# Kernel tuning notes

Hardware: AMD Instinct MI355X
Metric: run time of the kernel (lower is better)

Reference implementation:

```python
import jax, jax.numpy as jnp
import numpy as np

B, N, NB, E, H, A, K, D = 32, 512, 10, 1024, 256, 82, 4, 3


def setup_inputs() -> dict:
    key = jax.random.key(0)
    ks = iter(jax.random.split(key, 64))
    f = lambda shape: jax.random.normal(next(ks), shape, jnp.float32) * 0.05
    inp = {
        "atom_fea": jax.random.normal(next(ks), (B, N, A), jnp.float32),
        "bond_fea": jax.random.normal(next(ks), (B, E, 6), jnp.float32),
        "d_anb": jax.random.randint(next(ks), (B, N, NB), 0, N),
        "d_bnb": jax.random.randint(next(ks), (B, N, NB), 0, E),
        "d_nbs_mask": (jax.random.uniform(next(ks), (B, N, NB)) < 0.8).astype(jnp.float32),
        "d_mask": (jax.random.uniform(next(ks), (B, N)) < 0.9).astype(jnp.float32),
        "Wv": f((A, H)), "bv": f((H,)),
        "Wa_main": f((D, K, H, H)), "ba_main": f((D, K, H)),
        "Wa_super": f((D, K, H, H)), "ba_super": f((D, K, H)),
        "Wm": f((D, K, H, H)), "bm": f((D, K, H)),
        "Wbmm": f((D, K, H)), "bbmm": f((D, K)),
        "Wm2s": f((D, K * H, H)), "bm2s": f((D, H)),
        "Ws2m": f((D, H, H)), "bs2m": f((D, H)),
        "Wsup": f((D, H, H)), "bsup": f((D, H)),
        "Wzm1": f((D, H, H)), "bzm1": f((D, H)),
        "Wzm2": f((D, H, H)), "bzm2": f((D, H)),
        "Wzs1": f((D, H, H)), "bzs1": f((D, H)),
        "Wzs2": f((D, H, H)), "bzs2": f((D, H)),
        "Wu2": f((D, H + 6, H)), "bu2": f((D, H)),
        "Wu1": f((D, 2 * H, H)), "bu1": f((D, H)),
    }
    return inp


def mask_softmax(a, mask):
    a_max = jnp.max(a, -1, keepdims=True)
    e = jnp.exp(a - a_max) * mask
    return e / (jnp.sum(e, -1, keepdims=True) + 1e-6)


def _forward(atom_fea, bond_fea, d_nbs_mask, d_mask,
             Wv, bv, Wa_main, ba_main, Wa_super, ba_super, Wm, bm, Wbmm, bbmm,
             Wm2s, bm2s, Ws2m, bs2m, Wsup, bsup,
             Wzm1, bzm1, Wzm2, bzm2, Wzs1, bzs1, Wzs2, bzs2,
             Wu2, bu2, Wu1, bu1, d_anb, d_bnb):
    Bn = atom_fea.shape[0]
    bidx = jnp.arange(Bn)[:, None, None]
    # vertex embedding (default leaky_relu slope 0.01)
    vf = jax.nn.leaky_relu(atom_fea @ Wv + bv, 0.01)            # [B,N,H]
    sf = jnp.sum(vf * d_mask[:, :, None], axis=1, keepdims=True)  # [B,1,H]
    mask3 = d_nbs_mask[..., None]                               # [B,N,NB,1]
    for d in range(D):
        # --- multi-head main->super attention (vectorized over heads k) ---
        a_main = jnp.tanh(jnp.einsum('bnh,khj->bknj', vf, Wa_main[d]) + ba_main[d][None, :, None, :])
        a_super = jnp.tanh(jnp.einsum('boh,khj->bkoj', sf, Wa_super[d]) + ba_super[d][None, :, None, :])
        a = jnp.einsum('bknh,kh->bkn', a_main * a_super, Wbmm[d]) + bbmm[d][None, :, None]
        attn = mask_softmax(a, d_mask[:, None, :])               # [B,K,N]
        mvf = jnp.einsum('bnh,khj->bknj', vf, Wm[d]) + bm[d][None, :, None, :]
        m2s = jnp.einsum('bkn,bknh->bkh', attn, mvf).reshape(Bn, 1, K * H)
        main_to_super = jnp.tanh(m2s @ Wm2s[d] + bm2s[d])        # [B,1,H]
        # --- wln unit: gather neighbors, MLP, masked sum (slope 0.1) ---
        vnei = vf[bidx, d_anb]                                   # [B,N,NB,H]
        enei = bond_fea[bidx, d_bnb]                             # [B,N,NB,6]
        lnei = jnp.concatenate([vnei, enei], -1)                 # [B,N,NB,H+6]
        nei = jax.nn.leaky_relu(lnei @ Wu2[d] + bu2[d], 0.1)
        nei = jnp.sum(nei * mask3, axis=2)                       # [B,N,H]
        main_self = jax.nn.leaky_relu(jnp.concatenate([vf, nei], -1) @ Wu1[d] + bu1[d], 0.1)
        # --- GRU-style gated updates ---
        super_to_main = jnp.tanh(sf @ Ws2m[d] + bs2m[d])         # [B,1,H]
        super_self = jnp.tanh(sf @ Wsup[d] + bsup[d])            # [B,1,H]
        z_main = jax.nn.sigmoid(main_self @ Wzm1[d] + bzm1[d] + super_to_main @ Wzm2[d] + bzm2[d])
        vf = (1 - z_main) * main_self + z_main * super_to_main
        z_sup = jax.nn.sigmoid(super_self @ Wzs1[d] + bzs1[d] + main_to_super @ Wzs2[d] + bzs2[d])
        sf = (1 - z_sup) * super_self + z_sup * main_to_super    # [B,1,H]; sum over dim 1 is a no-op
    return vf, sf


def reference(atom_fea, bond_fea, d_anb, d_bnb, d_nbs_mask, d_mask,
              Wv, bv, Wa_main, ba_main, Wa_super, ba_super, Wm, bm, Wbmm, bbmm,
              Wm2s, bm2s, Ws2m, bs2m, Wsup, bsup,
              Wzm1, bzm1, Wzm2, bzm2, Wzs1, bzs1, Wzs2, bzs2,
              Wu2, bu2, Wu1, bu1):
    return _forward(atom_fea, bond_fea, d_nbs_mask, d_mask,
                    Wv, bv, Wa_main, ba_main, Wa_super, ba_super, Wm, bm, Wbmm, bbmm,
                    Wm2s, bm2s, Ws2m, bs2m, Wsup, bsup,
                    Wzm1, bzm1, Wzm2, bzm2, Wzs1, bzs1, Wzs2, bzs2,
                    Wu2, bu2, Wu1, bu1, d_anb, d_bnb)
```

## Files before the change

kernel.cpp:

```cpp
#include <hip/hip_runtime.h>
#include <hip/hip_bf16.h>

#define B_ 32
#define N_ 512
#define NB_ 10
#define E_ 1024
#define H_ 256
#define A_ 82
#define K_ 4
#define D_ 3
#define M_ (B_*N_)

typedef unsigned short u16;
typedef __attribute__((ext_vector_type(8))) short bf16x8;
typedef __attribute__((ext_vector_type(4))) float f32x4;

__device__ __forceinline__ float b2f(u16 u){
    unsigned int x = ((unsigned int)u) << 16;
    return __builtin_bit_cast(float, x);
}
__device__ __forceinline__ u16 f2b(float f){
    unsigned int x = __builtin_bit_cast(unsigned int, f);
    unsigned int lsb = (x >> 16) & 1u;
    x += 0x7fffu + lsb;
    return (u16)(x >> 16);
}
__device__ __forceinline__ float sigmoidf_(float x){ return 1.f/(1.f+expf(-x)); }

static constexpr int CVT_N[31] = {
    B_*E_*6, B_*N_*NB_, B_*N_,
    A_*H_, H_,
    D_*K_*H_*H_, D_*K_*H_, D_*K_*H_*H_, D_*K_*H_,
    D_*K_*H_*H_, D_*K_*H_, D_*K_*H_, D_*K_,
    D_*K_*H_*H_, D_*H_, D_*H_*H_, D_*H_,
    D_*H_*H_, D_*H_, D_*H_*H_, D_*H_,
    D_*H_*H_, D_*H_, D_*H_*H_, D_*H_,
    D_*H_*H_, D_*H_, D_*(H_+6)*H_, D_*H_,
    D_*2*H_*H_, D_*H_
};
struct Offs { long v[32]; };
static constexpr Offs mk_offs(){
    Offs o{}; o.v[0]=0;
    for(int i=0;i<31;i++) o.v[i+1]=o.v[i]+CVT_N[i];
    return o;
}
static constexpr Offs CVT_OFF = mk_offs();

struct Ptrs { const void* p[31]; };

__global__ void k_detect(const unsigned short* __restrict__ wv_raw, int* __restrict__ flag){
    float v = b2f(wv_raw[threadIdx.x]);
    bool plaus = (v==v) && (fabsf(v) < 100.0f);
    unsigned long long m = __ballot(plaus);
    if (threadIdx.x==0) *flag = (m == ~0ULL) ? 1 : 0;
}

__global__ void k_cvt(Ptrs ptrs, float* __restrict__ dst, const int* __restrict__ flag){
    int t = blockIdx.y;
    int n = CVT_N[t];
    int i4 = blockIdx.x*256 + threadIdx.x;
    if (i4*4 >= n) return;
    const void* src = ptrs.p[t];
    float4 o;
    if (*flag){
        ushort4 u = ((const ushort4*)src)[i4];
        o.x=b2f(u.x); o.y=b2f(u.y); o.z=b2f(u.z); o.w=b2f(u.w);
    } else {
        o = ((const float4*)src)[i4];
    }
    *(float4*)(dst + CVT_OFF.v[t] + (size_t)i4*4) = o;
}

__global__ void k_wt(const float* __restrict__ Wam, const float* __restrict__ Wu2,
                     const float* __restrict__ Wu1, const float* __restrict__ Wzm1,
                     u16* __restrict__ WT){
    int mi = blockIdx.z;
    const float* src;
    if (mi<12)      src = Wam  + (size_t)mi*H_*H_;
    else if (mi<15) src = Wu2  + (size_t)(mi-12)*(H_+6)*H_;
    else if (mi<18) src = Wu1  + (size_t)(mi-15)*2*H_*H_;
    else if (mi<21) src = Wu1  + (size_t)(mi-18)*2*H_*H_ + (size_t)H_*H_;
    else            src = Wzm1 + (size_t)(mi-21)*H_*H_;
    __shared__ float t[32][33];
    int x = threadIdx.x, y = threadIdx.y;
    int k0 = blockIdx.y*32, n0 = blockIdx.x*32;
    for(int yy=y; yy<32; yy+=8) t[yy][x] = src[(size_t)(k0+yy)*H_ + n0+x];
    __syncthreads();
    u16* dst = WT + ((size_t)mi*8 + (k0>>5))*(256*32);
    for(int yy=y; yy<32; yy+=8) dst[(size_t)(n0+yy)*32 + x] = f2b(t[x][yy]);
}

__global__ void k_embed(const u16* __restrict__ atom, const float* __restrict__ Wv,
                        const float* __restrict__ bv, u16* __restrict__ vfb,
                        const int* __restrict__ flag){
    __shared__ float arow[8][A_];
    int r0 = blockIdx.x*8; int j = threadIdx.x;
    int fl = *flag;
    for(int i=j;i<8*A_;i+=256){
        int r=i/A_, a=i-r*A_;
        arow[r][a] = fl ? b2f(atom[(size_t)(r0+r)*A_+a])
                        : ((const float*)atom)[(size_t)(r0+r)*A_+a];
    }
    __syncthreads();
    float acc[8];
    float bj = bv[j];
    #pragma unroll
    for(int r=0;r<8;r++) acc[r]=bj;
    for(int a=0;a<A_;a++){
        float w = Wv[a*H_+j];
        #pragma unroll
        for(int r=0;r<8;r++) acc[r] += arow[r][a]*w;
    }
    #pragma unroll
    for(int r=0;r<8;r++){
        float v = acc[r];
        vfb[(size_t)(r0+r)*H_+j] = f2b(v>0.f ? v : 0.01f*v);
    }
}

__global__ void k_sf0(const u16* __restrict__ vfb, const float* __restrict__ dmask,
                      float* __restrict__ sf){
    int b = blockIdx.x, h = threadIdx.x;
    __shared__ float mk[N_];
    for(int n=threadIdx.x;n<N_;n+=256) mk[n] = dmask[b*N_+n];
    __syncthreads();
    float s=0.f;
    #pragma unroll 8
    for(int n=0;n<N_;n++) s += mk[n]*b2f(vfb[((size_t)b*N_+n)*H_ + h]);
    sf[b*H_+h]=s;
}

__global__ void k_s1(int d, const float* __restrict__ sf,
    const float* __restrict__ Was, const float* __restrict__ bas,
    const float* __restrict__ Wbmm,
    const float* __restrict__ Ws2m, const float* __restrict__ bs2m,
    const float* __restrict__ Wsup, const float* __restrict__ bsup,
    float* __restrict__ asw, float* __restrict__ s2m, float* __restrict__ ssf)
{
    int b = blockIdx.x, m = blockIdx.y, j = threadIdx.x;
    __shared__ float sfl[H_];
    sfl[j] = sf[b*H_+j];
    __syncthreads();
    const float* W; float bias;
    if (m < 4){ W = Was + (size_t)(d*K_+m)*H_*H_; bias = bas[(d*K_+m)*H_+j]; }
    else if (m==4){ W = Ws2m + (size_t)d*H_*H_; bias = bs2m[d*H_+j]; }
    else { W = Wsup + (size_t)d*H_*H_; bias = bsup[d*H_+j]; }
    float acc = bias;
    #pragma unroll 8
    for(int h=0;h<H_;h++) acc += sfl[h]*W[h*H_+j];
    float v = tanhf(acc);
    if (m < 4) asw[(b*K_+m)*H_+j] = v * Wbmm[(d*K_+m)*H_+j];
    else if (m==4) s2m[b*H_+j] = v;
    else ssf[b*H_+j] = v;
}

__global__ void k_s2(int d, const float* __restrict__ s2m,
    const float* __restrict__ Wzm2, const float* __restrict__ bzm2,
    float* __restrict__ stm2p)
{
    int b=blockIdx.x, c=blockIdx.y, j=threadIdx.x;
    __shared__ float xl[64];
    if (j<64) xl[j] = s2m[b*H_ + c*64 + j];
    __syncthreads();
    const float* W = Wzm2 + (size_t)d*H_*H_ + (size_t)(c*64)*H_;
    float acc = (c==0) ? bzm2[d*H_+j] : 0.f;
    #pragma unroll 8
    for(int h=0;h<64;h++) acc += xl[h]*W[h*H_+j];
    stm2p[((size_t)c*B_+b)*H_+j] = acc;
}

__device__ __forceinline__ void mfma_core_bt(const u16* __restrict__ A,
    const u16* __restrict__ WTg, f32x4 acc[2][8],
    u16* __restrict__ Als, u16* __restrict__ Ws)
{
    const int LSA = 40, LSW = 40;
    int tid = threadIdx.x;
    int lane = tid & 63, wave = tid >> 6;
    int wy = wave >> 1, wx = wave & 1;
    int quad = lane >> 4, l15 = lane & 15;
    #pragma unroll
    for(int mt=0;mt<2;mt++)
        #pragma unroll
        for(int nt=0;nt<8;nt++) acc[mt][nt] = (f32x4){0.f,0.f,0.f,0.f};
    int arow = tid >> 2;
    int ak8  = (tid & 3) * 8;
    for(int k0=0;k0<H_;k0+=32){
        *(bf16x8*)(Als + arow*LSA + ak8) =
            *(const bf16x8*)(A + (size_t)arow*H_ + k0 + ak8);
        const u16* wsrc = WTg + (size_t)(k0>>5)*(256*32) + tid*32;
        #pragma unroll
        for(int c=0;c<4;c++)
            *(bf16x8*)(Ws + tid*LSW + c*8) = *(const bf16x8*)(wsrc + c*8);
        __syncthreads();
        bf16x8 af[2], bfr[8];
        #pragma unroll
        for(int mt=0;mt<2;mt++)
            af[mt] = *(const bf16x8*)(Als + (wy*32+mt*16+l15)*LSA + quad*8);
        #pragma unroll
        for(int nt=0;nt<8;nt++)
            bfr[nt] = *(const bf16x8*)(Ws + (wx*128+nt*16+l15)*LSW + quad*8);
        #pragma unroll
        for(int mt=0;mt<2;mt++)
            #pragma unroll
            for(int nt=0;nt<8;nt++)
                acc[mt][nt] = __builtin_amdgcn_mfma_f32_16x16x32_bf16(
                    af[mt], bfr[nt], acc[mt][nt], 0,0,0);
        __syncthreads();
    }
}

__global__ __launch_bounds__(256) void k_gemm_big(int d, const u16* __restrict__ vfb,
    const u16* __restrict__ WT, const float* __restrict__ ba_main,
    const float* __restrict__ bbmm, const float* __restrict__ bu1,
    const float* __restrict__ asw, float* __restrict__ score,
    u16* __restrict__ projb, float* __restrict__ pu1a)
{
    __shared__ u16 Als[64*40];
    __shared__ u16 Ws[256*40];
    __shared__ float sred[64][33];
    int m0 = blockIdx.x*64;
    int seg = blockIdx.y;
    int b = m0 >> 9;
    int mi;
    if (seg < 4)      mi = d*4+seg;
    else if (seg==4)  mi = 12+d;
    else              mi = 15+d;
    f32x4 acc[2][8];
    mfma_core_bt(vfb + (size_t)m0*H_, WT + (size_t)mi*H_*H_, acc, Als, Ws);
    int tid=threadIdx.x, lane=tid&63, wave=tid>>6;
    int wy=wave>>1, wx=wave&1, quad=lane>>4, l15=lane&15;
    if (seg < 4){
        const float* aswp = asw + (size_t)(b*K_+seg)*H_;
        const float* bap  = ba_main + (size_t)(d*K_+seg)*H_;
        float bbv[8], awv[8];
        #pragma unroll
        for(int nt=0;nt<8;nt++){
            int col = wx*128+nt*16+l15;
            bbv[nt]=bap[col]; awv[nt]=aswp[col];
        }
        #pragma unroll
        for(int mt=0;mt<2;mt++)
            #pragma unroll
            for(int r=0;r<4;r++){
                float p=0.f;
                #pragma unroll
                for(int nt=0;nt<8;nt++)
                    p += tanhf(acc[mt][nt][r]+bbv[nt])*awv[nt];
                int row = wy*32+mt*16+quad*4+r;
                sred[row][wx*16+l15] = p;
            }
        __syncthreads();
        if (tid < 64){
            float s=0.f;
            #pragma unroll 8
            for(int i=0;i<32;i++) s += sred[tid][i];
            score[(size_t)(b*K_+seg)*N_ + (m0&511) + tid] = s + bbmm[d*K_+seg];
        }
    } else if (seg==4){
        #pragma unroll
        for(int mt=0;mt<2;mt++)
            #pragma unroll
            for(int nt=0;nt<8;nt++){
                int col = wx*128+nt*16+l15;
                #pragma unroll
                for(int r=0;r<4;r++){
                    int row = m0 + wy*32+mt*16+quad*4+r;
                    projb[(size_t)row*H_+col] = f2b(acc[mt][nt][r]);
                }
            }
    } else {
        const float* bp = bu1 + d*H_;
        #pragma unroll
        for(int mt=0;mt<2;mt++)
            #pragma unroll
            for(int nt=0;nt<8;nt++){
                int col = wx*128+nt*16+l15;
                float bb = bp[col];
                #pragma unroll
                for(int r=0;r<4;r++){
                    int row = m0 + wy*32+mt*16+quad*4+r;
                    pu1a[(size_t)row*H_+col] = acc[mt][nt][r] + bb;
                }
            }
    }
}

__global__ __launch_bounds__(256) void k_mainself(int d, const u16* __restrict__ neib,
    const u16* __restrict__ WT, const float* __restrict__ pu1a, u16* __restrict__ msb)
{
    __shared__ u16 Als[64*40];
    __shared__ u16 Ws[256*40];
    int m0 = blockIdx.x*64;
    f32x4 acc[2][8];
    mfma_core_bt(neib + (size_t)m0*H_, WT + (size_t)(18+d)*H_*H_, acc, Als, Ws);
    int tid=threadIdx.x, lane=tid&63, wave=tid>>6;
    int wy=wave>>1, wx=wave&1, quad=lane>>4, l15=lane&15;
    #pragma unroll
    for(int mt=0;mt<2;mt++)
        #pragma unroll
        for(int nt=0;nt<8;nt++){
            int col = wx*128+nt*16+l15;
            #pragma unroll
            for(int r=0;r<4;r++){
                int row = m0 + wy*32+mt*16+quad*4+r;
                float v = acc[mt][nt][r] + pu1a[(size_t)row*H_+col];
                v = v>0.f? v : 0.1f*v;
                msb[(size_t)row*H_+col] = f2b(v);
            }
        }
}

__global__ __launch_bounds__(256) void k_update(int d, const u16* __restrict__ msb,
    const u16* __restrict__ WT, const float* __restrict__ bzm1,
    const float* __restrict__ stm2p, const float* __restrict__ s2m, u16* __restrict__ vfb)
{
    __shared__ u16 Als[64*40];
    __shared__ u16 Ws[256*40];
    int m0 = blockIdx.x*64; int b = m0>>9;
    f32x4 acc[2][8];
    mfma_core_bt(msb + (size_t)m0*H_, WT + (size_t)(21+d)*H_*H_, acc, Als, Ws);
    int tid=threadIdx.x, lane=tid&63, wave=tid>>6;
    int wy=wave>>1, wx=wave&1, quad=lane>>4, l15=lane&15;
    #pragma unroll
    for(int mt=0;mt<2;mt++)
        #pragma unroll
        for(int nt=0;nt<8;nt++){
            int col = wx*128+nt*16+l15;
            float bz = bzm1[d*H_+col];
            float st = stm2p[(size_t)(0*B_+b)*H_+col] + stm2p[(size_t)(1*B_+b)*H_+col]
                     + stm2p[(size_t)(2*B_+b)*H_+col] + stm2p[(size_t)(3*B_+b)*H_+col];
            float sm = s2m[b*H_+col];
            #pragma unroll
            for(int r=0;r<4;r++){
                int row = m0 + wy*32+mt*16+quad*4+r;
                float z = sigmoidf_(acc[mt][nt][r] + bz + st);
                float ms = b2f(msb[(size_t)row*H_+col]);
                vfb[(size_t)row*H_+col] = f2b((1.f-z)*ms + z*sm);
            }
        }
}

__global__ void k_softmax(float* __restrict__ score, const float* __restrict__ dmask,
                          float* __restrict__ sumattn){
    int b = blockIdx.x, k = blockIdx.y;
    int tid = threadIdx.x;
    __shared__ float sh[256];
    float* a = score + (size_t)(b*K_+k)*N_;
    float v0 = a[tid], v1 = a[tid+256];
    sh[tid]=fmaxf(v0,v1); __syncthreads();
    for(int s=128;s>0;s>>=1){ if(tid<s) sh[tid]=fmaxf(sh[tid],sh[tid+s]); __syncthreads(); }
    float m = sh[0]; __syncthreads();
    float e0 = expf(v0-m)*dmask[b*N_+tid], e1 = expf(v1-m)*dmask[b*N_+tid+256];
    sh[tid]=e0+e1; __syncthreads();
    for(int s=128;s>0;s>>=1){ if(tid<s) sh[tid]+=sh[tid+s]; __syncthreads(); }
    float S = sh[0];
    float inv = 1.f/(S+1e-6f);
    a[tid]=e0*inv; a[tid+256]=e1*inv;
    if(tid==0) sumattn[b*K_+k]=S*inv;
}

__global__ void k_t2(const float* __restrict__ attn, const u16* __restrict__ vfb,
                     float* __restrict__ tpart){
    int b=blockIdx.x, k=blockIdx.y, c=blockIdx.z, h=threadIdx.x;
    __shared__ float at[256];
    at[h] = attn[(size_t)(b*K_+k)*N_ + c*256 + h];
    __syncthreads();
    float acc=0.f;
    const u16* vfp = vfb + ((size_t)b*N_ + c*256)*H_ + h;
    #pragma unroll 8
    for(int n=0;n<256;n++) acc += at[n]*b2f(vfp[(size_t)n*H_]);
    tpart[((size_t)(c*B_+b)*K_+k)*H_+h]=acc;
}

__global__ void k_m1(int d, const float* __restrict__ tpart, const float* __restrict__ sumattn,
    const float* __restrict__ Wm, const float* __restrict__ bm, float* __restrict__ m2s)
{
    int b=blockIdx.x, k=blockIdx.y, j=threadIdx.x;
    __shared__ float tl[H_];
    tl[j] = tpart[((size_t)(0*B_+b)*K_+k)*H_+j] + tpart[((size_t)(1*B_+b)*K_+k)*H_+j];
    __syncthreads();
    const float* W = Wm + (size_t)(d*K_+k)*H_*H_;
    float acc = sumattn[b*K_+k]*bm[(d*K_+k)*H_+j];
    #pragma unroll 8
    for(int h=0;h<H_;h++) acc += tl[h]*W[h*H_+j];
    m2s[(size_t)(b*K_+k)*H_+j]=acc;
}

__global__ void k_m2(int d, const float* __restrict__ m2s, const float* __restrict__ Wm2s,
                     float* __restrict__ mtsp)
{
    int b=blockIdx.x, c=blockIdx.y, j=threadIdx.x;
    __shared__ float xl[H_];
    xl[j]=m2s[(size_t)(b*K_+c)*H_+j];
    __syncthreads();
    const float* W = Wm2s + (size_t)d*(K_*H_)*H_ + (size_t)(c*H_)*H_;
    float acc=0.f;
    #pragma unroll 8
    for(int h=0;h<H_;h++) acc += xl[h]*W[h*H_+j];
    mtsp[((size_t)c*B_+b)*H_+j]=acc;
}

__global__ void k_mts(int d, const float* __restrict__ mtsp, const float* __restrict__ bm2s,
                      float* __restrict__ mts){
    int b=blockIdx.x, j=threadIdx.x;
    float acc = bm2s[d*H_+j];
    #pragma unroll
    for(int c=0;c<4;c++) acc += mtsp[((size_t)c*B_+b)*H_+j];
    mts[b*H_+j]=tanhf(acc);
}

__global__ void k_m3(int d, const float* __restrict__ ssf, const float* __restrict__ mts,
    const float* __restrict__ Wzs1, const float* __restrict__ Wzs2,
    float* __restrict__ p1, float* __restrict__ p2)
{
    int b=blockIdx.x, m=blockIdx.y, j=threadIdx.x;
    __shared__ float xl[H_];
    const float* x = m ? mts : ssf;
    xl[j]=x[b*H_+j];
    __syncthreads();
    const float* W = (m ? Wzs2 : Wzs1) + (size_t)d*H_*H_;
    float acc=0.f;
    #pragma unroll 8
    for(int h=0;h<H_;h++) acc += xl[h]*W[h*H_+j];
    (m ? p2 : p1)[b*H_+j]=acc;
}

__global__ void k_sfup(int d, const float* __restrict__ p1, const float* __restrict__ p2,
    const float* __restrict__ bzs1, const float* __restrict__ bzs2,
    const float* __restrict__ ssf, const float* __restrict__ mts, float* __restrict__ sf)
{
    int b=blockIdx.x, j=threadIdx.x;
    float z = sigmoidf_(p1[b*H_+j]+bzs1[d*H_+j]+p2[b*H_+j]+bzs2[d*H_+j]);
    sf[b*H_+j]=(1.f-z)*ssf[b*H_+j]+z*mts[b*H_+j];
}

__global__ void k_nei(int d, const int* __restrict__ anb, const int* __restrict__ bnb,
    const float* __restrict__ nbm, const float* __restrict__ bond,
    const float* __restrict__ Wu2, const float* __restrict__ bu2,
    const u16* __restrict__ projb, u16* __restrict__ neib)
{
    __shared__ float W2s[6][256];
    __shared__ float bfeat[NB_][6];
    __shared__ int ai[NB_]; __shared__ int bi[NB_]; __shared__ float mk[NB_];
    int row = blockIdx.x; int b = row >> 9; int h = threadIdx.x;
    const float* W2 = Wu2 + (size_t)d*(H_+6)*H_ + (size_t)H_*H_;
    for(int i=h;i<6*H_;i+=256) W2s[i>>8][i&255] = W2[i];
    if (h<NB_){ ai[h]=anb[row*NB_+h]; bi[h]=bnb[row*NB_+h]; mk[h]=nbm[row*NB_+h]; }
    __syncthreads();
    if (h<NB_*6){ int jn=h/6, i=h-jn*6; bfeat[jn][i]=bond[((size_t)b*E_+bi[jn])*6+i]; }
    __syncthreads();
    float bu = bu2[d*H_+h];
    float acc=0.f;
    #pragma unroll
    for(int jn=0;jn<NB_;jn++){
        float v = b2f(projb[((size_t)b*N_+ai[jn])*H_+h]) + bu;
        #pragma unroll
        for(int i=0;i<6;i++) v += bfeat[jn][i]*W2s[i][h];
        v = v>0.f? v : 0.1f*v;
        acc += mk[jn]*v;
    }
    neib[(size_t)row*H_+h]=f2b(acc);
}

__global__ void k_out(const u16* __restrict__ vfb, const float* __restrict__ sf,
                      void* __restrict__ out, const int* __restrict__ flag){
    int idx = blockIdx.x*256 + threadIdx.x;
    const int total = M_*H_ + B_*H_;
    if (idx >= total) return;
    if (*flag){
        ((u16*)out)[idx] = (idx < M_*H_) ? vfb[idx] : f2b(sf[idx - M_*H_]);
    } else {
        ((float*)out)[idx] = (idx < M_*H_) ? b2f(vfb[idx]) : sf[idx - M_*H_];
    }
}

extern "C" void kernel_launch(void* const* d_in, const int* in_sizes, int n_in,
                              void* d_out, int out_size, void* d_ws, size_t ws_size,
                              hipStream_t stream)
{
    const int* anb = (const int*)d_in[2];
    const int* bnb = (const int*)d_in[3];

    float* ws   = (float*)d_ws;
    int*   flag = (int*)ws;
    float* cvt  = ws + 64;
    float* p    = cvt + ((CVT_OFF.v[31] + 63) & ~63L);
    float* pu1a      = p; p += (size_t)M_*H_;
    float* sf        = p; p += B_*H_;
    float* score     = p; p += B_*K_*N_;
    float* sumattn   = p; p += 128;
    float* asw       = p; p += B_*K_*H_;
    float* s2m       = p; p += B_*H_;
    float* ssf       = p; p += B_*H_;
    float* stm2p     = p; p += 4*B_*H_;
    float* tpart     = p; p += 2*B_*K_*H_;
    float* m2s       = p; p += B_*K_*H_;
    float* mtsp      = p; p += 4*B_*H_;
    float* mts       = p; p += B_*H_;
    float* p1        = p; p += B_*H_;
    float* p2        = p; p += B_*H_;
    u16*   WT        = (u16*)p;
    u16*   vfb       = WT  + (size_t)24*H_*H_;
    u16*   projb     = vfb + (size_t)M_*H_;
    u16*   neib     = projb + (size_t)M_*H_;
    u16*   msb      = neib  + (size_t)M_*H_;

    const float* cBond = cvt + CVT_OFF.v[0];
    const float* cNbm  = cvt + CVT_OFF.v[1];
    const float* cDm   = cvt + CVT_OFF.v[2];
    const float* cWv   = cvt + CVT_OFF.v[3];
    const float* cbv   = cvt + CVT_OFF.v[4];
    const float* cWam  = cvt + CVT_OFF.v[5];
    const float* cbam  = cvt + CVT_OFF.v[6];
    const float* cWas  = cvt + CVT_OFF.v[7];
    const float* cbas  = cvt + CVT_OFF.v[8];
    const float* cWm   = cvt + CVT_OFF.v[9];
    const float* cbm   = cvt + CVT_OFF.v[10];
    const float* cWbmm = cvt + CVT_OFF.v[11];
    const float* cbbmm = cvt + CVT_OFF.v[12];
    const float* cWm2s = cvt + CVT_OFF.v[13];
    const float* cbm2s = cvt + CVT_OFF.v[14];
    const float* cWs2m = cvt + CVT_OFF.v[15];
    const float* cbs2m = cvt + CVT_OFF.v[16];
    const float* cWsup = cvt + CVT_OFF.v[17];
    const float* cbsup = cvt + CVT_OFF.v[18];
    const float* cWzm1 = cvt + CVT_OFF.v[19];
    const float* cbzm1 = cvt + CVT_OFF.v[20];
    const float* cWzm2 = cvt + CVT_OFF.v[21];
    const float* cbzm2 = cvt + CVT_OFF.v[22];
    const float* cWzs1 = cvt + CVT_OFF.v[23];
    const float* cbzs1 = cvt + CVT_OFF.v[24];
    const float* cWzs2 = cvt + CVT_OFF.v[25];
    const float* cbzs2 = cvt + CVT_OFF.v[26];
    const float* cWu2  = cvt + CVT_OFF.v[27];
    const float* cbu2  = cvt + CVT_OFF.v[28];
    const float* cWu1  = cvt + CVT_OFF.v[29];
    const float* cbu1  = cvt + CVT_OFF.v[30];

    Ptrs ptrs;
    {
        int idx[31] = {1,4,5,6,7,8,9,10,11,12,13,14,15,16,17,18,19,20,21,
                       22,23,24,25,26,27,28,29,30,31,32,33};
        for(int i=0;i<31;i++) ptrs.p[i] = d_in[idx[i]];
    }

    k_detect<<<1,64,0,stream>>>((const unsigned short*)d_in[6], flag);
    {
        int maxv4 = (D_*K_*H_*H_ + 3)/4;
        int gx = (maxv4 + 255)/256;
        k_cvt<<<dim3(gx,31),256,0,stream>>>(ptrs, cvt, flag);
    }
    k_wt<<<dim3(8,8,24),dim3(32,8),0,stream>>>(cWam, cWu2, cWu1, cWzm1, WT);

    k_embed<<<M_/8,256,0,stream>>>((const u16*)d_in[0], cWv, cbv, vfb, flag);
    k_sf0<<<B_,256,0,stream>>>(vfb, cDm, sf);
    for(int d=0; d<D_; d++){
        k_s1<<<dim3(B_,6),256,0,stream>>>(d, sf, cWas, cbas, cWbmm,
                                          cWs2m, cbs2m, cWsup, cbsup, asw, s2m, ssf);
        k_s2<<<dim3(B_,4),256,0,stream>>>(d, s2m, cWzm2, cbzm2, stm2p);
        k_gemm_big<<<dim3(M_/64,6),256,0,stream>>>(d, vfb, WT, cbam, cbbmm, cbu1,
                                                   asw, score, projb, pu1a);
        k_softmax<<<dim3(B_,K_),256,0,stream>>>(score, cDm, sumattn);
        k_t2<<<dim3(B_,K_,2),256,0,stream>>>(score, vfb, tpart);
        k_m1<<<dim3(B_,K_),256,0,stream>>>(d, tpart, sumattn, cWm, cbm, m2s);
        k_m2<<<dim3(B_,4),256,0,stream>>>(d, m2s, cWm2s, mtsp);
        k_mts<<<B_,256,0,stream>>>(d, mtsp, cbm2s, mts);
        k_m3<<<dim3(B_,2),256,0,stream>>>(d, ssf, mts, cWzs1, cWzs2, p1, p2);
        k_sfup<<<B_,256,0,stream>>>(d, p1, p2, cbzs1, cbzs2, ssf, mts, sf);
        k_nei<<<M_,256,0,stream>>>(d, anb, bnb, cNbm, cBond, cWu2, cbu2, projb, neib);
        k_mainself<<<M_/64,256,0,stream>>>(d, neib, WT, pu1a, msb);
        k_update<<<M_/64,256,0,stream>>>(d, msb, WT, cbzm1, stm2p, s2m, vfb);
    }
    k_out<<<(M_*H_+B_*H_+255)/256,256,0,stream>>>(vfb, sf, d_out, flag);
}
```

Measured before the change: 804.5 us.

## Stage full A tile once, read weights from global, fuse super-node kernels

The shared MFMA GEMM core now loads the whole 64x256 A tile into LDS once and reads the pre-transposed weight fragments straight from global memory. This removes the per-k-step weight staging and both barriers inside the k-loop. Separately, the super-node chain (softmax, attention pooling, two matvecs, tanh, gate) is merged from seven launches into three, cutting launch overhead and intermediate buffers. Weight reads from global depend on cache hits, and the attention pooling now uses fewer blocks (each loops over all 512 nodes), which lowers parallelism.

```diff
diff --git a/kernel.cpp b/kernel.cpp
--- a/kernel.cpp
+++ b/kernel.cpp
@@ -169,11 +169,10 @@
     stm2p[((size_t)c*B_+b)*H_+j] = acc;
 }
 
-__device__ __forceinline__ void mfma_core_bt(const u16* __restrict__ A,
-    const u16* __restrict__ WTg, f32x4 acc[2][8],
-    u16* __restrict__ Als, u16* __restrict__ Ws)
-{
-    const int LSA = 40, LSW = 40;
+#define LSA_ 264
+__device__ __forceinline__ void mfma_core_v2(const u16* __restrict__ A,
+    const u16* __restrict__ WTg, f32x4 acc[2][8], u16* __restrict__ Als)
+{
     int tid = threadIdx.x;
     int lane = tid & 63, wave = tid >> 6;
     int wy = wave >> 1, wx = wave & 1;
@@ -183,29 +182,28 @@
         #pragma unroll
         for(int nt=0;nt<8;nt++) acc[mt][nt] = (f32x4){0.f,0.f,0.f,0.f};
     int arow = tid >> 2;
-    int ak8  = (tid & 3) * 8;
+    int ac   = (tid & 3) * 8;
+    #pragma unroll
+    for(int c=0;c<8;c++)
+        *(bf16x8*)(Als + arow*LSA_ + ac + c*32) =
+            *(const bf16x8*)(A + (size_t)arow*H_ + ac + c*32);
+    __syncthreads();
+    #pragma unroll
     for(int k0=0;k0<H_;k0+=32){
-        *(bf16x8*)(Als + arow*LSA + ak8) =
-            *(const bf16x8*)(A + (size_t)arow*H_ + k0 + ak8);
-        const u16* wsrc = WTg + (size_t)(k0>>5)*(256*32) + tid*32;
-        #pragma unroll
-        for(int c=0;c<4;c++)
-            *(bf16x8*)(Ws + tid*LSW + c*8) = *(const bf16x8*)(wsrc + c*8);
-        __syncthreads();
         bf16x8 af[2], bfr[8];
         #pragma unroll
         for(int mt=0;mt<2;mt++)
-            af[mt] = *(const bf16x8*)(Als + (wy*32+mt*16+l15)*LSA + quad*8);
+            af[mt] = *(const bf16x8*)(Als + (wy*32+mt*16+l15)*LSA_ + k0 + quad*8);
+        const u16* wsrc = WTg + (size_t)(k0>>5)*(256*32);
         #pragma unroll
         for(int nt=0;nt<8;nt++)
-            bfr[nt] = *(const bf16x8*)(Ws + (wx*128+nt*16+l15)*LSW + quad*8);
+            bfr[nt] = *(const bf16x8*)(wsrc + (wx*128+nt*16+l15)*32 + quad*8);
         #pragma unroll
         for(int mt=0;mt<2;mt++)
             #pragma unroll
             for(int nt=0;nt<8;nt++)
                 acc[mt][nt] = __builtin_amdgcn_mfma_f32_16x16x32_bf16(
                     af[mt], bfr[nt], acc[mt][nt], 0,0,0);
-        __syncthreads();
     }
 }
 
@@ -215,8 +213,7 @@
     const float* __restrict__ asw, float* __restrict__ score,
     u16* __restrict__ projb, float* __restrict__ pu1a)
 {
-    __shared__ u16 Als[64*40];
-    __shared__ u16 Ws[256*40];
+    __shared__ u16 Als[64*LSA_];
     __shared__ float sred[64][33];
     int m0 = blockIdx.x*64;
     int seg = blockIdx.y;
@@ -226,7 +223,7 @@
     else if (seg==4)  mi = 12+d;
     else              mi = 15+d;
     f32x4 acc[2][8];
-    mfma_core_bt(vfb + (size_t)m0*H_, WT + (size_t)mi*H_*H_, acc, Als, Ws);
+    mfma_core_v2(vfb + (size_t)m0*H_, WT + (size_t)mi*H_*H_, acc, Als);
     int tid=threadIdx.x, lane=tid&63, wave=tid>>6;
     int wy=wave>>1, wx=wave&1, quad=lane>>4, l15=lane&15;
     if (seg < 4){
@@ -288,11 +285,10 @@
 __global__ __launch_bounds__(256) void k_mainself(int d, const u16* __restrict__ neib,
     const u16* __restrict__ WT, const float* __restrict__ pu1a, u16* __restrict__ msb)
 {
-    __shared__ u16 Als[64*40];
-    __shared__ u16 Ws[256*40];
+    __shared__ u16 Als[64*LSA_];
     int m0 = blockIdx.x*64;
     f32x4 acc[2][8];
-    mfma_core_bt(neib + (size_t)m0*H_, WT + (size_t)(18+d)*H_*H_, acc, Als, Ws);
+    mfma_core_v2(neib + (size_t)m0*H_, WT + (size_t)(18+d)*H_*H_, acc, Als);
     int tid=threadIdx.x, lane=tid&63, wave=tid>>6;
     int wy=wave>>1, wx=wave&1, quad=lane>>4, l15=lane&15;
     #pragma unroll
@@ -314,11 +310,10 @@
     const u16* __restrict__ WT, const float* __restrict__ bzm1,
     const float* __restrict__ stm2p, const float* __restrict__ s2m, u16* __restrict__ vfb)
 {
-    __shared__ u16 Als[64*40];
-    __shared__ u16 Ws[256*40];
+    __shared__ u16 Als[64*LSA_];
     int m0 = blockIdx.x*64; int b = m0>>9;
     f32x4 acc[2][8];
-    mfma_core_bt(msb + (size_t)m0*H_, WT + (size_t)(21+d)*H_*H_, acc, Als, Ws);
+    mfma_core_v2(msb + (size_t)m0*H_, WT + (size_t)(21+d)*H_*H_, acc, Als);
     int tid=threadIdx.x, lane=tid&63, wave=tid>>6;
     int wy=wave>>1, wx=wave&1, quad=lane>>4, l15=lane&15;
     #pragma unroll
@@ -340,12 +335,14 @@
         }
 }
 
-__global__ void k_softmax(float* __restrict__ score, const float* __restrict__ dmask,
-                          float* __restrict__ sumattn){
+__global__ void k_attn(const float* __restrict__ score, const float* __restrict__ dmask,
+                       const u16* __restrict__ vfb, float* __restrict__ tbuf,
+                       float* __restrict__ sumattn){
     int b = blockIdx.x, k = blockIdx.y;
     int tid = threadIdx.x;
     __shared__ float sh[256];
-    float* a = score + (size_t)(b*K_+k)*N_;
+    __shared__ float at[N_];
+    const float* a = score + (size_t)(b*K_+k)*N_;
     float v0 = a[tid], v1 = a[tid+256];
     sh[tid]=fmaxf(v0,v1); __syncthreads();
     for(int s=128;s>0;s>>=1){ if(tid<s) sh[tid]=fmaxf(sh[tid],sh[tid+s]); __syncthreads(); }
@@ -355,83 +352,66 @@
     for(int s=128;s>0;s>>=1){ if(tid<s) sh[tid]+=sh[tid+s]; __syncthreads(); }
     float S = sh[0];
     float inv = 1.f/(S+1e-6f);
-    a[tid]=e0*inv; a[tid+256]=e1*inv;
+    at[tid]=e0*inv; at[tid+256]=e1*inv;
     if(tid==0) sumattn[b*K_+k]=S*inv;
-}
-
-__global__ void k_t2(const float* __restrict__ attn, const u16* __restrict__ vfb,
-                     float* __restrict__ tpart){
-    int b=blockIdx.x, k=blockIdx.y, c=blockIdx.z, h=threadIdx.x;
-    __shared__ float at[256];
-    at[h] = attn[(size_t)(b*K_+k)*N_ + c*256 + h];
     __syncthreads();
     float acc=0.f;
-    const u16* vfp = vfb + ((size_t)b*N_ + c*256)*H_ + h;
+    const u16* vfp = vfb + (size_t)b*N_*H_ + tid;
     #pragma unroll 8
-    for(int n=0;n<256;n++) acc += at[n]*b2f(vfp[(size_t)n*H_]);
-    tpart[((size_t)(c*B_+b)*K_+k)*H_+h]=acc;
-}
-
-__global__ void k_m1(int d, const float* __restrict__ tpart, const float* __restrict__ sumattn,
-    const float* __restrict__ Wm, const float* __restrict__ bm, float* __restrict__ m2s)
+    for(int n=0;n<N_;n++) acc += at[n]*b2f(vfp[(size_t)n*H_]);
+    tbuf[(size_t)(b*K_+k)*H_+tid]=acc;
+}
+
+__global__ void k_m12(int d, const float* __restrict__ tbuf, const float* __restrict__ sumattn,
+    const float* __restrict__ Wm, const float* __restrict__ bm,
+    const float* __restrict__ Wm2s, float* __restrict__ mtsp)
 {
     int b=blockIdx.x, k=blockIdx.y, j=threadIdx.x;
     __shared__ float tl[H_];
-    tl[j] = tpart[((size_t)(0*B_+b)*K_+k)*H_+j] + tpart[((size_t)(1*B_+b)*K_+k)*H_+j];
-    __syncthreads();
-    const float* W = Wm + (size_t)(d*K_+k)*H_*H_;
-    float acc = sumattn[b*K_+k]*bm[(d*K_+k)*H_+j];
-    #pragma unroll 8
-    for(int h=0;h<H_;h++) acc += tl[h]*W[h*H_+j];
-    m2s[(size_t)(b*K_+k)*H_+j]=acc;
-}
-
-__global__ void k_m2(int d, const float* __restrict__ m2s, const float* __restrict__ Wm2s,
-                     float* __restrict__ mtsp)
-{
-    int b=blockIdx.x, c=blockIdx.y, j=threadIdx.x;
-    __shared__ float xl[H_];
-    xl[j]=m2s[(size_t)(b*K_+c)*H_+j];
-    __syncthreads();
-    const float* W = Wm2s + (size_t)d*(K_*H_)*H_ + (size_t)(c*H_)*H_;
-    float acc=0.f;
-    #pragma unroll 8
-    for(int h=0;h<H_;h++) acc += xl[h]*W[h*H_+j];
-    mtsp[((size_t)c*B_+b)*H_+j]=acc;
-}
-
-__global__ void k_mts(int d, const float* __restrict__ mtsp, const float* __restrict__ bm2s,
-                      float* __restrict__ mts){
+    __shared__ float m2sl[H_];
+    tl[j] = tbuf[(size_t)(b*K_+k)*H_+j];
+    __syncthreads();
+    {
+        const float* W = Wm + (size_t)(d*K_+k)*H_*H_;
+        float acc = sumattn[b*K_+k]*bm[(d*K_+k)*H_+j];
+        #pragma unroll 8
+        for(int h=0;h<H_;h++) acc += tl[h]*W[h*H_+j];
+        m2sl[j]=acc;
+    }
+    __syncthreads();
+    {
+        const float* W = Wm2s + (size_t)d*(K_*H_)*H_ + (size_t)(k*H_)*H_;
+        float acc=0.f;
+        #pragma unroll 8
+        for(int h=0;h<H_;h++) acc += m2sl[h]*W[h*H_+j];
+        mtsp[((size_t)k*B_+b)*H_+j]=acc;
+    }
+}
+
+__global__ void k_sftail(int d, const float* __restrict__ mtsp, const float* __restrict__ bm2s,
+    const float* __restrict__ ssf,
+    const float* __restrict__ Wzs1, const float* __restrict__ bzs1,
+    const float* __restrict__ Wzs2, const float* __restrict__ bzs2,
+    float* __restrict__ sf)
+{
     int b=blockIdx.x, j=threadIdx.x;
-    float acc = bm2s[d*H_+j];
-    #pragma unroll
-    for(int c=0;c<4;c++) acc += mtsp[((size_t)c*B_+b)*H_+j];
-    mts[b*H_+j]=tanhf(acc);
-}
-
-__global__ void k_m3(int d, const float* __restrict__ ssf, const float* __restrict__ mts,
-    const float* __restrict__ Wzs1, const float* __restrict__ Wzs2,
-    float* __restrict__ p1, float* __restrict__ p2)
-{
-    int b=blockIdx.x, m=blockIdx.y, j=threadIdx.x;
-    __shared__ float xl[H_];
-    const float* x = m ? mts : ssf;
-    xl[j]=x[b*H_+j];
-    __syncthreads();
-    const float* W = (m ? Wzs2 : Wzs1) + (size_t)d*H_*H_;
-    float acc=0.f;
-    #pragma unroll 8
-    for(int h=0;h<H_;h++) acc += xl[h]*W[h*H_+j];
-    (m ? p2 : p1)[b*H_+j]=acc;
-}
-
-__global__ void k_sfup(int d, const float* __restrict__ p1, const float* __restrict__ p2,
-    const float* __restrict__ bzs1, const float* __restrict__ bzs2,
-    const float* __restrict__ ssf, const float* __restrict__ mts, float* __restrict__ sf)
-{
-    int b=blockIdx.x, j=threadIdx.x;
-    float z = sigmoidf_(p1[b*H_+j]+bzs1[d*H_+j]+p2[b*H_+j]+bzs2[d*H_+j]);
-    sf[b*H_+j]=(1.f-z)*ssf[b*H_+j]+z*mts[b*H_+j];
+    __shared__ float mtsl[H_];
+    __shared__ float ssl[H_];
+    {
+        float acc = bm2s[d*H_+j];
+        #pragma unroll
+        for(int c=0;c<4;c++) acc += mtsp[((size_t)c*B_+b)*H_+j];
+        mtsl[j]=tanhf(acc);
+        ssl[j]=ssf[b*H_+j];
+    }
+    __syncthreads();
+    const float* W1 = Wzs1 + (size_t)d*H_*H_;
+    const float* W2 = Wzs2 + (size_t)d*H_*H_;
+    float acc = bzs1[d*H_+j] + bzs2[d*H_+j];
+    #pragma unroll 4
+    for(int h=0;h<H_;h++) acc += ssl[h]*W1[h*H_+j] + mtsl[h]*W2[h*H_+j];
+    float z = sigmoidf_(acc);
+    sf[b*H_+j]=(1.f-z)*ssl[j]+z*mtsl[j];
 }
 
 __global__ void k_nei(int d, const int* __restrict__ anb, const int* __restrict__ bnb,
@@ -493,17 +473,13 @@
     float* s2m       = p; p += B_*H_;
     float* ssf       = p; p += B_*H_;
     float* stm2p     = p; p += 4*B_*H_;
-    float* tpart     = p; p += 2*B_*K_*H_;
-    float* m2s       = p; p += B_*K_*H_;
+    float* tbuf      = p; p += B_*K_*H_;
     float* mtsp      = p; p += 4*B_*H_;
-    float* mts       = p; p += B_*H_;
-    float* p1        = p; p += B_*H_;
-    float* p2        = p; p += B_*H_;
     u16*   WT        = (u16*)p;
     u16*   vfb       = WT  + (size_t)24*H_*H_;
     u16*   projb     = vfb + (size_t)M_*H_;
-    u16*   neib     = projb + (size_t)M_*H_;
-    u16*   msb      = neib  + (size_t)M_*H_;
+    u16*   neib      = projb + (size_t)M_*H_;
+    u16*   msb       = neib  + (size_t)M_*H_;
 
     const float* cBond = cvt + CVT_OFF.v[0];
     const float* cNbm  = cvt + CVT_OFF.v[1];
@@ -560,13 +536,10 @@
         k_s2<<<dim3(B_,4),256,0,stream>>>(d, s2m, cWzm2, cbzm2, stm2p);
         k_gemm_big<<<dim3(M_/64,6),256,0,stream>>>(d, vfb, WT, cbam, cbbmm, cbu1,
                                                    asw, score, projb, pu1a);
-        k_softmax<<<dim3(B_,K_),256,0,stream>>>(score, cDm, sumattn);
-        k_t2<<<dim3(B_,K_,2),256,0,stream>>>(score, vfb, tpart);
-        k_m1<<<dim3(B_,K_),256,0,stream>>>(d, tpart, sumattn, cWm, cbm, m2s);
-        k_m2<<<dim3(B_,4),256,0,stream>>>(d, m2s, cWm2s, mtsp);
-        k_mts<<<B_,256,0,stream>>>(d, mtsp, cbm2s, mts);
-        k_m3<<<dim3(B_,2),256,0,stream>>>(d, ssf, mts, cWzs1, cWzs2, p1, p2);
-        k_sfup<<<B_,256,0,stream>>>(d, p1, p2, cbzs1, cbzs2, ssf, mts, sf);
+        k_attn<<<dim3(B_,K_),256,0,stream>>>(score, cDm, vfb, tbuf, sumattn);
+        k_m12<<<dim3(B_,K_),256,0,stream>>>(d, tbuf, sumattn, cWm, cbm, cWm2s, mtsp);
+        k_sftail<<<B_,256,0,stream>>>(d, mtsp, cbm2s, ssf, cWzs1, cbzs1,
+                                      cWzs2, cbzs2, sf);
         k_nei<<<M_,256,0,stream>>>(d, anb, bnb, cNbm, cBond, cWu2, cbu2, projb, neib);
         k_mainself<<<M_/64,256,0,stream>>>(d, neib, WT, pu1a, msb);
         k_update<<<M_/64,256,0,stream>>>(d, msb, WT, cbzm1, stm2p, s2m, vfb);
```

Result: slower. 848.8 us (+5.5%).
